# Kernel tuning notes

Hardware: AMD Instinct MI355X
Metric: run time of the kernel (lower is better)

Reference implementation:

```python
import jax, jax.numpy as jnp
import numpy as np

# Dimensions: B=batch, T=timesteps, D=input_dim, U=units, R=recurrent_size, NE=#edge types
B, T, D, U, R, NE = 1024, 128, 256, 256, 4, 40


def setup_inputs() -> dict:
    key = jax.random.key(0)
    ks = jax.random.split(key, 11)
    s = 1.0 / np.sqrt(U)  # RandomUniform(-1/sqrt(units), 1/sqrt(units)) as in __init__
    inputs = jax.random.normal(ks[0], (B, T, D), jnp.float32)
    input_lengths = jax.random.randint(ks[1], (B,), 1, T + 1)
    # dependencies[b, t, k] indexes a PAST timestep (< t) whose hidden state feeds step t;
    # values >= t are treated as '$' (no dependency -> zero state), matching the string-'$' logic.
    dependencies = jax.random.randint(ks[2], (B, T, R - 1), 0, T)
    edge_types = jax.random.randint(ks[3], (B, T, R), 0, NE)
    mask = jax.random.randint(ks[4], (B, T), 0, 2).astype(bool)
    cell_mask = jax.random.randint(ks[5], (B, T, R), 0, 2).astype(bool)
    Wx = jax.random.uniform(ks[6], (D, 3 * U), jnp.float32, -s, s)   # input kernel (r,z,h)
    Uh = jax.random.uniform(ks[7], (U, 3 * U), jnp.float32, -s, s)   # recurrent kernel (r,z,h)
    Ve = jax.random.uniform(ks[8], (U, 3 * U), jnp.float32, -s, s)   # edge-embedding kernel (r,z,h)
    b = jax.random.uniform(ks[9], (3 * U,), jnp.float32, -s, s)
    edge_emb = jax.random.normal(ks[10], (NE, U), jnp.float32) * 0.02  # shared_emb table
    return dict(inputs=inputs, input_lengths=input_lengths, dependencies=dependencies,
                edge_types=edge_types, mask=mask, cell_mask=cell_mask,
                Wx=Wx, Uh=Uh, Ve=Ve, b=b, edge_emb=edge_emb)


def _graph_gru_forward(inputs, dependencies, edge_types, mask, cell_mask, Wx, Uh, Ve, b, edge_emb):
    Bn, Tn, Dn = inputs.shape
    Un = Uh.shape[0]
    # time-major, as the wrapper does with swap_batch_timestep
    xg_t = jnp.einsum('btd,dg->tbg', inputs, Wx) + b   # precompute input projections [T,B,3U]
    dep_t = jnp.swapaxes(dependencies, 0, 1)           # [T,B,R-1]
    et_t = jnp.swapaxes(edge_types, 0, 1)              # [T,B,R]
    m_t = jnp.swapaxes(mask, 0, 1)                     # [T,B]
    cm_t = jnp.swapaxes(cell_mask, 0, 1)               # [T,B,R]
    bidx = jnp.arange(Bn)

    def step(carry, xs):
        h_prev, H = carry                  # h_prev: [B,U]; H: running history of states [T,B,U]
        t, xg, dep, et, m, cm = xs
        # gather dependency states from history; dep >= t means '$' -> zero state
        valid = dep < t                                        # [B,R-1]
        dep_states = H[jnp.clip(dep, 0, Tn - 1), bidx[:, None]]  # [B,R-1,U]
        dep_states = jnp.where(valid[..., None], dep_states, 0.0)
        hs = jnp.concatenate([h_prev[:, None, :], dep_states], axis=1)  # states tuple -> [B,R,U]
        cmf = cm.astype(hs.dtype)[..., None]                   # per-slot cell mask [B,R,1]
        hs_m = hs * cmf
        e_m = edge_emb[et] * cmf                               # [B,R,U]
        # aggregate messages from the R masked (state, edge-embedding) slots into the 3 gates
        msg = jnp.einsum('bru,ug->bg', hs_m, Uh) + jnp.einsum('bru,ug->bg', e_m, Ve)  # [B,3U]
        xr, xz, xh = jnp.split(xg, 3, axis=-1)
        mr, mz, mh = jnp.split(msg, 3, axis=-1)
        r = jax.nn.sigmoid(xr + mr)
        z = jax.nn.sigmoid(xz + mz)
        hcand = jnp.tanh(xh + r * mh)
        denom = jnp.maximum(cmf.sum(axis=1), 1.0)              # [B,1]
        h_bar = hs_m.sum(axis=1) / denom                       # mean of active predecessor states
        h_new = z * h_bar + (1.0 - z) * hcand
        # masked update: where(mask_t, new_state, previous return state)
        h_out = jnp.where(m[:, None], h_new, h_prev)
        H = H.at[t].set(h_out)
        return (h_out, H), None

    h0 = jnp.zeros((Bn, Un), inputs.dtype)
    H0 = jnp.zeros((Tn, Bn, Un), inputs.dtype)
    (h_last, _), _ = jax.lax.scan(
        step, (h0, H0), (jnp.arange(Tn), xg_t, dep_t, et_t, m_t, cm_t))
    # zero_output_for_mask on the last output (return_sequences=False)
    return jnp.where(m_t[-1][:, None], h_last, 0.0)


def reference(inputs, input_lengths, dependencies, edge_types, mask, cell_mask,
              Wx, Uh, Ve, b, edge_emb):
    # input_lengths only matters when go_backwards=True (default False) -> unused.
    del input_lengths
    return _graph_gru_forward(inputs, dependencies, edge_types, mask, cell_mask,
                              Wx, Uh, Ve, b, edge_emb)
```

## Files before the change

kernel.cpp:

```cpp
#include <hip/hip_runtime.h>
#include <hip/hip_bf16.h>
#include <stdint.h>

typedef _Float16 f16;
typedef _Float16 f16x8 __attribute__((ext_vector_type(8)));
typedef _Float16 f16x4 __attribute__((ext_vector_type(4)));
typedef float    f32x4 __attribute__((ext_vector_type(4)));

#define B_N 1024
#define T_N 128
#define U_N 256
#define G3  768
#define NC  1024
#define KC  512
#define M_N (B_N * T_N)
#define S16P 264

__device__ __forceinline__ void glds16(const void* g, void* l) {
  __builtin_amdgcn_global_load_lds((const __attribute__((address_space(1))) unsigned int*)g,
                                   (__attribute__((address_space(3))) unsigned int*)l, 16, 0, 0);
}
__device__ __forceinline__ void glds4(const void* g, void* l) {
  __builtin_amdgcn_global_load_lds((const __attribute__((address_space(1))) unsigned int*)g,
                                   (__attribute__((address_space(3))) unsigned int*)l, 4, 0, 0);
}

__global__ void k_prep(const float* __restrict__ Wx, const float* __restrict__ Uh,
                       const float* __restrict__ Ve, const float* __restrict__ bsrc,
                       f16* __restrict__ B2, float* __restrict__ bias, f16* __restrict__ UhF)
{
  int idx = blockIdx.x * 256 + threadIdx.x;
  if (idx < NC * KC) {
    int e = idx & 7, slot = (idx >> 3) & 3, r = (idx >> 5) & 127;
    int kt = (idx >> 12) & 15, nt8 = idx >> 16;
    int swz = ((r >> 2) ^ r) & 3;
    int np = nt8 * 128 + r;
    int k  = kt * 32 + ((slot ^ swz) & 3) * 8 + e;
    int u = np >> 2, part = np & 3;
    float v;
    if (part == 0)      v = (k < 256) ? Wx[k * G3 + u]         : Ve[(k - 256) * G3 + u];
    else if (part == 1) v = (k < 256) ? Wx[k * G3 + 256 + u]   : Ve[(k - 256) * G3 + 256 + u];
    else if (part == 2) v = (k < 256) ? Wx[k * G3 + 512 + u]   : 0.f;
    else                v = (k < 256) ? 0.f                    : Ve[(k - 256) * G3 + 512 + u];
    B2[idx] = (f16)v;
    return;
  }
  int i2 = idx - NC * KC;
  if (i2 < U_N * G3) {
    int j = i2 & 7, lane = (i2 >> 3) & 63, fn = i2 >> 9;
    int nt = fn % 6, kkw = fn / 6;
    int kk = kkw & 7, w = kkw >> 3;
    int k = kk * 32 + (lane >> 4) * 8 + j;
    int npp = w * 96 + nt * 16 + (lane & 15);
    int q = npp >> 4;
    int u = (q / 3) * 16 + (npp & 15), gate = q % 3;
    UhF[i2] = (f16)Uh[k * G3 + gate * 256 + u];
    return;
  }
  int i3 = i2 - U_N * G3;
  if (i3 < NC) {
    int u = i3 >> 2, part = i3 & 3;
    bias[i3] = (part < 3) ? bsrc[part * 256 + u] : 0.f;
  }
}

__global__ __launch_bounds__(256) void k_build_a2(const float* __restrict__ inp, const int* __restrict__ et,
                           const int* __restrict__ cmk, const float* __restrict__ emb,
                           f16* __restrict__ A2)
{
  int idx = blockIdx.x * 256 + threadIdx.x;
  int slot = idx & 3, t = (idx >> 2) & 127, kt = (idx >> 9) & 15, b = idx >> 13;
  int swz = ((t >> 2) ^ t) & 3;
  int k0 = kt * 32 + ((slot ^ swz) & 3) * 8;
  int m = b * 128 + t;
  f16x8 v;
  if (k0 < 256) {
    const float* s = inp + (size_t)m * 256 + k0;
    #pragma unroll
    for (int j = 0; j < 8; ++j) v[j] = (f16)s[j];
  } else {
    int c = k0 - 256;
    const int* e  = et  + (size_t)m * 4;
    const int* cm = cmk + (size_t)m * 4;
    float a[8] = {0,0,0,0,0,0,0,0};
    #pragma unroll
    for (int r = 0; r < 4; ++r)
      if (cm[r]) {
        const float* es = emb + e[r] * U_N + c;
        #pragma unroll
        for (int j = 0; j < 8; ++j) a[j] += es[j];
      }
    #pragma unroll
    for (int j = 0; j < 8; ++j) v[j] = (f16)a[j];
  }
  *(f16x8*)(A2 + (size_t)idx * 8) = v;
}

__global__ __launch_bounds__(256) void k_gemm2(const f16* __restrict__ A2,
                                               const f16* __restrict__ B2,
                                               const float* __restrict__ bias,
                                               f16* __restrict__ C)
{
  __shared__ __align__(16) f16 sbuf[3][2][4096];
  const int tid  = threadIdx.x;
  const int lane = tid & 63, wv = tid >> 6;
  const int wm = wv >> 1, wn = wv & 1;
  const int l15 = lane & 15, lhi = lane >> 4;
  const int wg = (blockIdx.x & 7) * 1024 + (blockIdx.x >> 3);
  const int mt = wg >> 3, nt = wg & 7;
  const int m0 = mt * 128, n0 = nt * 128;

  const f16* gabase = A2 + (size_t)mt * 16 * 4096 + wv * 1024 + lane * 8;
  const f16* gbbase = B2 + (size_t)nt * 16 * 4096 + wv * 1024 + lane * 8;

  #define STAGE(kt_, buf_) do {                                             \
    int kk_ = (kt_);                                                        \
    glds16(gabase + (size_t)kk_ * 4096,       &sbuf[buf_][0][wv * 1024]);   \
    glds16(gabase + (size_t)kk_ * 4096 + 512, &sbuf[buf_][0][wv * 1024 + 512]); \
    glds16(gbbase + (size_t)kk_ * 4096,       &sbuf[buf_][1][wv * 1024]);   \
    glds16(gbbase + (size_t)kk_ * 4096 + 512, &sbuf[buf_][1][wv * 1024 + 512]); \
  } while (0)

  f32x4 acc[4][4] = {};

  STAGE(0, 0);
  STAGE(1, 1);
  __builtin_amdgcn_sched_barrier(0);

  int aoff[4], boff[4];
  #pragma unroll
  for (int i = 0; i < 4; ++i) {
    int ar = wm * 64 + i * 16 + l15;
    aoff[i] = ar * 32 + ((lhi ^ ((ar >> 2) ^ ar)) & 3) * 8;
    int br = wn * 64 + i * 16 + l15;
    boff[i] = br * 32 + ((lhi ^ ((br >> 2) ^ br)) & 3) * 8;
  }

  for (int t = 0; t < 16; ++t) {
    const int buf  = t % 3;
    const int bufp = (t + 2) % 3;
    STAGE((t + 2 < 16) ? (t + 2) : 15, bufp);
    __builtin_amdgcn_sched_barrier(0);
    asm volatile("s_waitcnt vmcnt(8)" ::: "memory");
    __builtin_amdgcn_sched_barrier(0);
    __builtin_amdgcn_s_barrier();
    __builtin_amdgcn_sched_barrier(0);

    const f16* sA = &sbuf[buf][0][0];
    const f16* sB = &sbuf[buf][1][0];
    f16x8 af[4], bf[4];
    #pragma unroll
    for (int i = 0; i < 4; ++i) {
      af[i] = *(const f16x8*)(sA + aoff[i]);
      bf[i] = *(const f16x8*)(sB + boff[i]);
    }
    __builtin_amdgcn_s_setprio(1);
    #pragma unroll
    for (int i = 0; i < 4; ++i)
      #pragma unroll
      for (int j = 0; j < 4; ++j)
        acc[i][j] = __builtin_amdgcn_mfma_f32_16x16x32_f16(af[i], bf[j], acc[i][j], 0, 0, 0);
    __builtin_amdgcn_s_setprio(0);

    asm volatile("s_waitcnt lgkmcnt(0)" ::: "memory");
    __builtin_amdgcn_s_barrier();
    __builtin_amdgcn_sched_barrier(0);
  }

  float bv[4];
  #pragma unroll
  for (int j = 0; j < 4; ++j) bv[j] = bias[n0 + wn * 64 + j * 16 + l15];
  asm volatile("s_waitcnt vmcnt(0)" ::: "memory");
  __builtin_amdgcn_sched_barrier(0);
  __builtin_amdgcn_s_barrier();

  f16* ep = &sbuf[0][0][0];
  #pragma unroll
  for (int i = 0; i < 4; ++i)
    #pragma unroll
    for (int j = 0; j < 4; ++j)
      #pragma unroll
      for (int r = 0; r < 4; ++r)
        ep[(wm * 64 + i * 16 + lhi * 4 + r) * 132 + wn * 64 + j * 16 + l15] =
            (f16)(acc[i][j][r] + bv[j]);
  __syncthreads();

  #pragma unroll
  for (int it = 0; it < 8; ++it) {
    int row = it * 16 + (tid >> 4), chunk = tid & 15;
    *(f16x8*)(C + (size_t)(m0 + row) * 1024 + n0 + chunk * 8) =
        *(const f16x8*)(ep + row * 132 + chunk * 8);
  }
  #undef STAGE
}

__global__ __launch_bounds__(512, 2) void k_scan4(
    const f16* __restrict__ pre,
    const f16* __restrict__ UhF,
    const int* __restrict__ dep,
    const int* __restrict__ cmk,
    const int* __restrict__ msk,
    f16* __restrict__ H16,
    float* __restrict__ out)
{
  __shared__ __align__(16) f16 s16[16 * S16P];
  __shared__ __align__(16) f16 hring[2][1024];
  __shared__ __align__(16) f16 dbuf[2][3072];
  __shared__ __align__(16) f16 spre[3][4096];
  __shared__ __align__(16) int sidxl[4][64];
  __shared__ __align__(16) int dpad[64];

  const int tid  = threadIdx.x;
  const int lane = tid & 63, w = tid >> 6;
  const int l15  = lane & 15, lhi = lane >> 4;
  const int b0   = blockIdx.x * 4;

  f16x8 uh[48];
  {
    const f16* ub = UhF + ((size_t)w * 48 * 64 + lane) * 8;
    #pragma unroll
    for (int i = 0; i < 48; ++i) uh[i] = *(const f16x8*)(ub + i * 512);
    #pragma unroll
    for (int i = 0; i < 32; ++i) asm volatile("" : "+v"(uh[i]));
  }

  ((int*)hring)[tid]       = 0;
  ((int*)hring)[tid + 512] = 0;

  if (tid < 96) {
    int tt = tid >> 5, ll2 = tid & 31, rr = ll2 >> 3, f = ll2 & 7;
    size_t b = b0 + rr;
    int v;
    if (f < 4)      v = cmk[(b * T_N + tt) * 4 + f];
    else if (f < 7) v = dep[(b * T_N + tt) * 3 + (f - 4)];
    else            v = msk[b * T_N + tt];
    sidxl[tt][rr * 8 + f] = v;
  }
  __syncthreads();

  const f16* spre_src = pre + ((size_t)(b0 + (w >> 1)) * T_N) * 1024 + (w & 1) * 512 + lane * 8;
  const int  ll = lane & 31;
  const int  srr = ll >> 3, sf = ll & 7;
  const size_t sb = b0 + srr;
  const int* sidx_base;
  int sidx_stride;
  if (sf < 4)      { sidx_base = cmk + sb * T_N * 4 + sf;       sidx_stride = 4; }
  else if (sf < 7) { sidx_base = dep + sb * T_N * 3 + (sf - 4); sidx_stride = 3; }
  else             { sidx_base = msk + sb * T_N;                sidx_stride = 1; }
  const int dq  = 2 * w + (lane >> 5);
  const int drr = dq / 3, drm = dq - drr * 3;
  const f16* dsrc_base = H16 + (size_t)(b0 + drr) * 256 + (lane & 31) * 8;
  const int strr = ((w - 6) * 64 + lane) >> 5;
  const int stuo = (((w - 6) * 64 + lane) & 31) * 8;

  #pragma unroll
  for (int pr = 0; pr < 2; ++pr)
    glds16(spre_src + (size_t)pr * 1024, &spre[pr][w * 512]);
  #pragma unroll
  for (int i = 0; i < 3; ++i)
    glds4(msk, &dpad[0]);

  for (int t = 0; t < T_N; ++t) {
    asm volatile("s_waitcnt vmcnt(2)" ::: "memory");
    __builtin_amdgcn_sched_barrier(0);

    if (tid < 128) {
      const int rr = tid >> 5, uo = (tid & 31) * 8;
      const int* six = &sidxl[t & 3][rr * 8];
      int cm0 = six[0];
      int cms0 = six[1], cms1 = six[2], cms2 = six[3];
      int dd0 = six[4],  dd1 = six[5],  dd2 = six[6];
      f16x8 hprev = *(const f16x8*)&hring[(t + 1) & 1][rr * 256 + uo];
      f16x8 hold  = *(const f16x8*)&hring[t & 1][rr * 256 + uo];
      f32x4 a0 = {0.f,0.f,0.f,0.f}, a1 = {0.f,0.f,0.f,0.f};
      if (cm0) {
        #pragma unroll
        for (int j = 0; j < 4; ++j) { a0[j] += (float)hprev[j]; a1[j] += (float)hprev[j + 4]; }
      }
      int cma[3] = {cms0, cms1, cms2};
      int dda[3] = {dd0, dd1, dd2};
      #pragma unroll
      for (int r = 0; r < 3; ++r) {
        f16x8 dv = *(const f16x8*)&dbuf[t & 1][(rr * 3 + r) * 256 + uo];
        int d = dda[r];
        f16x8 src = (d == t - 1) ? hprev : ((d == t - 2) ? hold : dv);
        if (cma[r] && (d < t)) {
          #pragma unroll
          for (int j = 0; j < 4; ++j) { a0[j] += (float)src[j]; a1[j] += (float)src[j + 4]; }
        }
      }
      f16x8 s8;
      #pragma unroll
      for (int j = 0; j < 4; ++j) { s8[j] = (f16)a0[j]; s8[j + 4] = (f16)a1[j]; }
      *(f16x8*)&s16[(rr * 4) * S16P + uo] = s8;
    }
    asm volatile("s_waitcnt lgkmcnt(0)" ::: "memory");
    __builtin_amdgcn_s_barrier();
    __builtin_amdgcn_sched_barrier(0);

    if (w < 6) {
      int d = sidxl[(t + 1) & 3][drr * 8 + 4 + drm];
      glds16(dsrc_base + (size_t)d * (B_N * 256), &dbuf[(t + 1) & 1][w * 512]);
    } else {
      f16x8 hv = *(const f16x8*)&hring[(t + 1) & 1][strr * 256 + stuo];
      int tt = (t == 0) ? T_N : (t - 1);
      *(f16x8*)(H16 + ((size_t)tt * B_N + b0 + strr) * 256 + stuo) = hv;
    }
    __builtin_amdgcn_sched_barrier(0);
    {
      int tt2 = (t + 2 < T_N) ? (t + 2) : (T_N - 1);
      glds16(spre_src + (size_t)tt2 * 1024, &spre[(t + 2) % 3][w * 512]);
    }
    __builtin_amdgcn_sched_barrier(0);
    {
      int t3 = (t + 3 < T_N) ? (t + 3) : (T_N - 1);
      glds4(sidx_base + (size_t)t3 * sidx_stride, &sidxl[(t + 3) & 3][0]);
    }
    __builtin_amdgcn_sched_barrier(0);

    f32x4 acc[6];
    #pragma unroll
    for (int i = 0; i < 6; ++i) acc[i] = (f32x4){0.f, 0.f, 0.f, 0.f};
    __builtin_amdgcn_s_setprio(1);
    #pragma unroll
    for (int kk = 0; kk < 8; ++kk) {
      f16x8 a = *(const f16x8*)(s16 + l15 * S16P + kk * 32 + lhi * 8);
      #pragma unroll
      for (int nt = 0; nt < 6; ++nt)
        acc[nt] = __builtin_amdgcn_mfma_f32_16x16x32_f16(a, uh[kk * 6 + nt], acc[nt], 0, 0, 0);
    }
    __builtin_amdgcn_s_setprio(0);

    asm volatile("s_waitcnt vmcnt(7)" ::: "memory");
    __builtin_amdgcn_sched_barrier(0);
    {
      const int* six = &sidxl[t & 3][lhi * 8];
      int c0 = six[0], c1 = six[1], c2 = six[2], c3 = six[3];
      int mfl = six[7];
      float cnt  = (float)(c0 + c1 + c2 + c3);
      float rcnt = __builtin_amdgcn_rcpf(fmaxf(cnt, 1.f));
      #pragma unroll
      for (int ub2 = 0; ub2 < 2; ++ub2) {
        int u = w * 32 + ub2 * 16 + l15;
        f16x4 p = *(const f16x4*)&spre[t % 3][lhi * 1024 + u * 4];
        float mr = acc[ub2 * 3 + 0][0];
        float mz = acc[ub2 * 3 + 1][0];
        float mh = acc[ub2 * 3 + 2][0];
        float tr = (float)p.x + mr;
        float tz = (float)p.y + mz;
        float hx = (float)p.z;
        float he = (float)p.w;
        float rg = __builtin_amdgcn_rcpf(1.f + __expf(-tr));
        float zg = __builtin_amdgcn_rcpf(1.f + __expf(-tz));
        float aa = hx + rg * (mh + he);
        float hc = 2.f * __builtin_amdgcn_rcpf(1.f + __expf(-2.f * aa)) - 1.f;
        float sv = (float)s16[(lhi * 4) * S16P + u];
        float hb = sv * rcnt;
        float hn = zg * hb + (1.f - zg) * hc;
        float hp_ = (float)hring[(t + 1) & 1][lhi * 256 + u];
        float ho = mfl ? hn : hp_;
        hring[t & 1][lhi * 256 + u] = (f16)ho;
      }
    }
    asm volatile("s_waitcnt lgkmcnt(0)" ::: "memory");
    __builtin_amdgcn_s_barrier();
    __builtin_amdgcn_sched_barrier(0);
  }

  if (tid < 128) {
    const int rr = tid >> 5, uo = (tid & 31) * 8;
    int m = sidxl[(T_N - 1) & 3][rr * 8 + 7];
    f16x8 h8 = *(const f16x8*)&hring[(T_N - 1) & 1][rr * 256 + uo];
    f32x4 o0, o1;
    #pragma unroll
    for (int j = 0; j < 4; ++j) {
      o0[j] = m ? (float)h8[j]     : 0.f;
      o1[j] = m ? (float)h8[j + 4] : 0.f;
    }
    *(f32x4*)(out + (size_t)(b0 + rr) * 256 + uo)     = o0;
    *(f32x4*)(out + (size_t)(b0 + rr) * 256 + uo + 4) = o1;
  }
}

extern "C" void kernel_launch(void* const* d_in, const int* in_sizes, int n_in,
                              void* d_out, int out_size, void* d_ws, size_t ws_size,
                              hipStream_t stream)
{
  const float* inputs = (const float*)d_in[0];
  const int*   deps   = (const int*)d_in[2];
  const int*   et     = (const int*)d_in[3];
  const int*   msk    = (const int*)d_in[4];
  const int*   cmk    = (const int*)d_in[5];
  const float* Wx     = (const float*)d_in[6];
  const float* Uh     = (const float*)d_in[7];
  const float* Ve     = (const float*)d_in[8];
  const float* bb     = (const float*)d_in[9];
  const float* emb    = (const float*)d_in[10];
  float* out = (float*)d_out;

  char* ws = (char*)d_ws;
  f16*   A2    = (f16*)ws;
  f16*   H16   = (f16*)ws;
  f16*   pre   = (f16*)(ws + 134217728);
  f16*   B2    = (f16*)(ws + 402653184);
  float* bias  = (float*)(ws + 403701760);
  f16*   UhF   = (f16*)(ws + 403705856);

  int prep_n = NC * KC + U_N * G3 + NC;
  k_prep<<<dim3((prep_n + 255) / 256), dim3(256), 0, stream>>>(Wx, Uh, Ve, bb, B2, bias, UhF);
  k_build_a2<<<dim3(M_N * 64 / 256), dim3(256), 0, stream>>>(inputs, et, cmk, emb, A2);
  k_gemm2<<<dim3((M_N / 128) * (NC / 128)), dim3(256), 0, stream>>>(A2, B2, bias, pre);
  k_scan4<<<dim3(B_N / 4), dim3(512), 0, stream>>>(pre, UhF, deps, cmk, msk, H16, out);
}
```

Baseline: 506.1 us.

## Process sixteen batch rows per scan block to fill all MFMA rows

The recurrent scan kernel now handles 16 batch rows per block instead of 4, so every row of the 16x16 MFMA tile carries real data and the register-resident Uh weights are reused across four times as many sequences. Gate math loops over four accumulator rows, and the pre-activation prefetch moves from triple to double buffering with per-step loads of the dependency history, indices and inputs all reorganised. The grid shrinks to 64 blocks, which leaves most compute units idle, and LDS use per block grows substantially.

```diff
diff --git a/kernel.cpp b/kernel.cpp
--- a/kernel.cpp
+++ b/kernel.cpp
@@ -194,7 +194,7 @@
   #undef STAGE
 }
 
-__global__ __launch_bounds__(512, 2) void k_scan4(
+__global__ __launch_bounds__(512, 2) void k_scan8(
     const f16* __restrict__ pre,
     const f16* __restrict__ UhF,
     const int* __restrict__ dep,
@@ -204,72 +204,62 @@
     float* __restrict__ out)
 {
   __shared__ __align__(16) f16 s16[16 * S16P];
-  __shared__ __align__(16) f16 hring[2][1024];
-  __shared__ __align__(16) f16 dbuf[2][3072];
-  __shared__ __align__(16) f16 spre[3][4096];
-  __shared__ __align__(16) int sidxl[4][64];
-  __shared__ __align__(16) int dpad[64];
+  __shared__ __align__(16) f16 hring[2][4096];
+  __shared__ __align__(16) f16 dbuf[2][12288];
+  __shared__ __align__(16) f16 spre[2][16384];
+  __shared__ int sidxl[4][16][8];
+  __shared__ int dpad[64];
 
   const int tid  = threadIdx.x;
   const int lane = tid & 63, w = tid >> 6;
   const int l15  = lane & 15, lhi = lane >> 4;
-  const int b0   = blockIdx.x * 4;
+  const int b0   = blockIdx.x * 16;
 
   f16x8 uh[48];
   {
     const f16* ub = UhF + ((size_t)w * 48 * 64 + lane) * 8;
     #pragma unroll
     for (int i = 0; i < 48; ++i) uh[i] = *(const f16x8*)(ub + i * 512);
-    #pragma unroll
-    for (int i = 0; i < 32; ++i) asm volatile("" : "+v"(uh[i]));
-  }
-
-  ((int*)hring)[tid]       = 0;
-  ((int*)hring)[tid + 512] = 0;
-
-  if (tid < 96) {
-    int tt = tid >> 5, ll2 = tid & 31, rr = ll2 >> 3, f = ll2 & 7;
+  }
+
+  for (int i = tid; i < 4096; i += 512) ((int*)hring)[i] = 0;
+
+  if (tid < 384) {
+    int tt = tid >> 7, ll2 = tid & 127, rr = ll2 >> 3, f = ll2 & 7;
     size_t b = b0 + rr;
     int v;
     if (f < 4)      v = cmk[(b * T_N + tt) * 4 + f];
     else if (f < 7) v = dep[(b * T_N + tt) * 3 + (f - 4)];
     else            v = msk[b * T_N + tt];
-    sidxl[tt][rr * 8 + f] = v;
+    sidxl[tt][rr][f] = v;
   }
   __syncthreads();
-
-  const f16* spre_src = pre + ((size_t)(b0 + (w >> 1)) * T_N) * 1024 + (w & 1) * 512 + lane * 8;
-  const int  ll = lane & 31;
-  const int  srr = ll >> 3, sf = ll & 7;
-  const size_t sb = b0 + srr;
-  const int* sidx_base;
-  int sidx_stride;
-  if (sf < 4)      { sidx_base = cmk + sb * T_N * 4 + sf;       sidx_stride = 4; }
-  else if (sf < 7) { sidx_base = dep + sb * T_N * 3 + (sf - 4); sidx_stride = 3; }
-  else             { sidx_base = msk + sb * T_N;                sidx_stride = 1; }
-  const int dq  = 2 * w + (lane >> 5);
-  const int drr = dq / 3, drm = dq - drr * 3;
-  const f16* dsrc_base = H16 + (size_t)(b0 + drr) * 256 + (lane & 31) * 8;
-  const int strr = ((w - 6) * 64 + lane) >> 5;
-  const int stuo = (((w - 6) * 64 + lane) & 31) * 8;
-
+  __builtin_amdgcn_sched_barrier(0);
+
+  const size_t prow0 = ((size_t)(b0 + 2 * w) * T_N) * 1024 + lane * 8;
+  const size_t prow1 = ((size_t)(b0 + 2 * w + 1) * T_N) * 1024 + lane * 8;
+  const int srow = 2 * w + (lane >> 5);
+  const int soff = (lane & 31) * 8;
+  const int lh32 = lane >> 5;
+
+  glds16(pre + prow0,       &spre[0][(2 * w) * 1024]);
+  glds16(pre + prow0 + 512, &spre[0][(2 * w) * 1024 + 512]);
+  glds16(pre + prow1,       &spre[0][(2 * w + 1) * 1024]);
+  glds16(pre + prow1 + 512, &spre[0][(2 * w + 1) * 1024 + 512]);
   #pragma unroll
-  for (int pr = 0; pr < 2; ++pr)
-    glds16(spre_src + (size_t)pr * 1024, &spre[pr][w * 512]);
-  #pragma unroll
-  for (int i = 0; i < 3; ++i)
-    glds4(msk, &dpad[0]);
+  for (int i = 0; i < 5; ++i) glds4(msk, &dpad[0]);
+  __builtin_amdgcn_sched_barrier(0);
 
   for (int t = 0; t < T_N; ++t) {
-    asm volatile("s_waitcnt vmcnt(2)" ::: "memory");
-    __builtin_amdgcn_sched_barrier(0);
-
-    if (tid < 128) {
+    asm volatile("s_waitcnt vmcnt(1)" ::: "memory");
+    __builtin_amdgcn_sched_barrier(0);
+
+    {
       const int rr = tid >> 5, uo = (tid & 31) * 8;
-      const int* six = &sidxl[t & 3][rr * 8];
+      const int* six = &sidxl[t & 3][rr][0];
       int cm0 = six[0];
-      int cms0 = six[1], cms1 = six[2], cms2 = six[3];
-      int dd0 = six[4],  dd1 = six[5],  dd2 = six[6];
+      int cma[3] = {six[1], six[2], six[3]};
+      int dda[3] = {six[4], six[5], six[6]};
       f16x8 hprev = *(const f16x8*)&hring[(t + 1) & 1][rr * 256 + uo];
       f16x8 hold  = *(const f16x8*)&hring[t & 1][rr * 256 + uo];
       f32x4 a0 = {0.f,0.f,0.f,0.f}, a1 = {0.f,0.f,0.f,0.f};
@@ -277,8 +267,6 @@
         #pragma unroll
         for (int j = 0; j < 4; ++j) { a0[j] += (float)hprev[j]; a1[j] += (float)hprev[j + 4]; }
       }
-      int cma[3] = {cms0, cms1, cms2};
-      int dda[3] = {dd0, dd1, dd2};
       #pragma unroll
       for (int r = 0; r < 3; ++r) {
         f16x8 dv = *(const f16x8*)&dbuf[t & 1][(rr * 3 + r) * 256 + uo];
@@ -292,29 +280,50 @@
       f16x8 s8;
       #pragma unroll
       for (int j = 0; j < 4; ++j) { s8[j] = (f16)a0[j]; s8[j + 4] = (f16)a1[j]; }
-      *(f16x8*)&s16[(rr * 4) * S16P + uo] = s8;
+      *(f16x8*)&s16[rr * S16P + uo] = s8;
     }
     asm volatile("s_waitcnt lgkmcnt(0)" ::: "memory");
     __builtin_amdgcn_s_barrier();
     __builtin_amdgcn_sched_barrier(0);
 
-    if (w < 6) {
-      int d = sidxl[(t + 1) & 3][drr * 8 + 4 + drm];
-      glds16(dsrc_base + (size_t)d * (B_N * 256), &dbuf[(t + 1) & 1][w * 512]);
+    {
+      size_t tt = (size_t)((t + 1 < T_N) ? (t + 1) : (T_N - 1)) * 1024;
+      const int sl = (t + 1) & 1;
+      glds16(pre + prow0 + tt,       &spre[sl][(2 * w) * 1024]);
+      glds16(pre + prow0 + tt + 512, &spre[sl][(2 * w) * 1024 + 512]);
+      glds16(pre + prow1 + tt,       &spre[sl][(2 * w + 1) * 1024]);
+      glds16(pre + prow1 + tt + 512, &spre[sl][(2 * w + 1) * 1024 + 512]);
+    }
+    __builtin_amdgcn_sched_barrier(0);
+    {
+      f16x8 hv = *(const f16x8*)&hring[(t + 1) & 1][srow * 256 + soff];
+      int tts = (t == 0) ? T_N : (t - 1);
+      *(f16x8*)(H16 + ((size_t)tts * B_N + b0 + srow) * 256 + soff) = hv;
+    }
+    __builtin_amdgcn_sched_barrier(0);
+    {
+      int tn = (t + 1 < T_N) ? (t + 1) : (T_N - 1);
+      #pragma unroll
+      for (int i = 0; i < 3; ++i) {
+        int v = 2 * (3 * w + i) + lh32;
+        int drr = v / 3, drm = v - 3 * drr;
+        int d = sidxl[tn & 3][drr][4 + drm];
+        const f16* src = H16 + (size_t)d * (B_N * 256) + (size_t)(b0 + drr) * 256 + soff;
+        glds16(src, &dbuf[(t + 1) & 1][(2 * (3 * w + i)) * 256]);
+      }
+    }
+    __builtin_amdgcn_sched_barrier(0);
+    if (w < 2) {
+      int t3 = (t + 3 < T_N) ? (t + 3) : (T_N - 1);
+      int f0 = w * 64 + lane, rr = f0 >> 3, f = f0 & 7;
+      size_t b = b0 + rr;
+      const int* src;
+      if (f < 4)      src = cmk + (b * T_N + t3) * 4 + f;
+      else if (f < 7) src = dep + (b * T_N + t3) * 3 + (f - 4);
+      else            src = msk + b * T_N + t3;
+      glds4(src, (int*)&sidxl[t3 & 3][0][0] + w * 64);
     } else {
-      f16x8 hv = *(const f16x8*)&hring[(t + 1) & 1][strr * 256 + stuo];
-      int tt = (t == 0) ? T_N : (t - 1);
-      *(f16x8*)(H16 + ((size_t)tt * B_N + b0 + strr) * 256 + stuo) = hv;
-    }
-    __builtin_amdgcn_sched_barrier(0);
-    {
-      int tt2 = (t + 2 < T_N) ? (t + 2) : (T_N - 1);
-      glds16(spre_src + (size_t)tt2 * 1024, &spre[(t + 2) % 3][w * 512]);
-    }
-    __builtin_amdgcn_sched_barrier(0);
-    {
-      int t3 = (t + 3 < T_N) ? (t + 3) : (T_N - 1);
-      glds4(sidx_base + (size_t)t3 * sidx_stride, &sidxl[(t + 3) & 3][0]);
+      glds4(msk, &dpad[0]);
     }
     __builtin_amdgcn_sched_barrier(0);
 
@@ -331,10 +340,10 @@
     }
     __builtin_amdgcn_s_setprio(0);
 
-    asm volatile("s_waitcnt vmcnt(7)" ::: "memory");
-    __builtin_amdgcn_sched_barrier(0);
-    {
-      const int* six = &sidxl[t & 3][lhi * 8];
+    #pragma unroll
+    for (int r = 0; r < 4; ++r) {
+      const int row = lhi * 4 + r;
+      const int* six = &sidxl[t & 3][row][0];
       int c0 = six[0], c1 = six[1], c2 = six[2], c3 = six[3];
       int mfl = six[7];
       float cnt  = (float)(c0 + c1 + c2 + c3);
@@ -342,10 +351,10 @@
       #pragma unroll
       for (int ub2 = 0; ub2 < 2; ++ub2) {
         int u = w * 32 + ub2 * 16 + l15;
-        f16x4 p = *(const f16x4*)&spre[t % 3][lhi * 1024 + u * 4];
-        float mr = acc[ub2 * 3 + 0][0];
-        float mz = acc[ub2 * 3 + 1][0];
-        float mh = acc[ub2 * 3 + 2][0];
+        f16x4 p = *(const f16x4*)&spre[t & 1][row * 1024 + u * 4];
+        float mr = acc[ub2 * 3 + 0][r];
+        float mz = acc[ub2 * 3 + 1][r];
+        float mh = acc[ub2 * 3 + 2][r];
         float tr = (float)p.x + mr;
         float tz = (float)p.y + mz;
         float hx = (float)p.z;
@@ -354,12 +363,12 @@
         float zg = __builtin_amdgcn_rcpf(1.f + __expf(-tz));
         float aa = hx + rg * (mh + he);
         float hc = 2.f * __builtin_amdgcn_rcpf(1.f + __expf(-2.f * aa)) - 1.f;
-        float sv = (float)s16[(lhi * 4) * S16P + u];
+        float sv = (float)s16[row * S16P + u];
         float hb = sv * rcnt;
         float hn = zg * hb + (1.f - zg) * hc;
-        float hp_ = (float)hring[(t + 1) & 1][lhi * 256 + u];
+        float hp_ = (float)hring[(t + 1) & 1][row * 256 + u];
         float ho = mfl ? hn : hp_;
-        hring[t & 1][lhi * 256 + u] = (f16)ho;
+        hring[t & 1][row * 256 + u] = (f16)ho;
       }
     }
     asm volatile("s_waitcnt lgkmcnt(0)" ::: "memory");
@@ -367,9 +376,9 @@
     __builtin_amdgcn_sched_barrier(0);
   }
 
-  if (tid < 128) {
+  {
     const int rr = tid >> 5, uo = (tid & 31) * 8;
-    int m = sidxl[(T_N - 1) & 3][rr * 8 + 7];
+    int m = sidxl[(T_N - 1) & 3][rr][7];
     f16x8 h8 = *(const f16x8*)&hring[(T_N - 1) & 1][rr * 256 + uo];
     f32x4 o0, o1;
     #pragma unroll
@@ -410,5 +419,5 @@
   k_prep<<<dim3((prep_n + 255) / 256), dim3(256), 0, stream>>>(Wx, Uh, Ve, bb, B2, bias, UhF);
   k_build_a2<<<dim3(M_N * 64 / 256), dim3(256), 0, stream>>>(inputs, et, cmk, emb, A2);
   k_gemm2<<<dim3((M_N / 128) * (NC / 128)), dim3(256), 0, stream>>>(A2, B2, bias, pre);
-  k_scan4<<<dim3(B_N / 4), dim3(512), 0, stream>>>(pre, UhF, deps, cmk, msk, H16, out);
-}
+  k_scan8<<<dim3(B_N / 16), dim3(512), 0, stream>>>(pre, UhF, deps, cmk, msk, H16, out);
+}
```

Result: slower. 993.0 us (+96.2%).
